# Performance work log

Hardware: AMD Instinct MI355X
Metric: run time of the kernel (lower is better)

The kernel has to match this reference:

```python
import jax, jax.numpy as jnp
import numpy as np

B, SQ, SKV, D = 8, 2048, 2048, 1024

def setup_inputs() -> dict:
    key = jax.random.key(0)
    ks = jax.random.split(key, 8)
    s = 1.0 / np.sqrt(D)  # torch Linear default init range
    return {
        "target": jax.random.normal(ks[0], (B, SQ, D), dtype=jnp.float32),
        "non_target": jax.random.normal(ks[1], (B, SKV, D), dtype=jnp.float32),
        "Wq": jax.random.uniform(ks[2], (D, D), jnp.float32, -s, s),
        "bq": jax.random.uniform(ks[3], (D,), jnp.float32, -s, s),
        "Wk": jax.random.uniform(ks[4], (D, D), jnp.float32, -s, s),
        "bk": jax.random.uniform(ks[5], (D,), jnp.float32, -s, s),
        "Wv": jax.random.uniform(ks[6], (D, D), jnp.float32, -s, s),
        "bv": jax.random.uniform(ks[7], (D,), jnp.float32, -s, s),
    }

def reference(target, non_target, Wq, bq, Wk, bk, Wv, bv):
    # Linear projections (torch Linear: x @ W.T + b)
    q = jnp.einsum('bsd,ed->bse', target, Wq) + bq       # [B,SQ,D]
    k = jnp.einsum('bsd,ed->bse', non_target, Wk) + bk   # [B,SKV,D]
    v = jnp.einsum('bsd,ed->bse', non_target, Wv) + bv   # [B,SKV,D]
    # Unscaled attention, exactly as the original module (no 1/sqrt(d))
    scores = jnp.einsum('bqd,bkd->bqk', q, k)            # [B,SQ,SKV]
    weights = jax.nn.softmax(scores, axis=-1)
    return jnp.einsum('bqk,bkd->bqd', weights, v)        # [B,SQ,D]
```

## Files before the change

kernel.cpp:

```cpp
#include <hip/hip_runtime.h>


typedef _Float16 half8 __attribute__((ext_vector_type(8)));
typedef _Float16 half4v __attribute__((ext_vector_type(4)));
typedef float floatx4 __attribute__((ext_vector_type(4)));

__device__ __forceinline__ void async_copy16(const _Float16* g, _Float16* l) {
  __builtin_amdgcn_global_load_lds(
      (const __attribute__((address_space(1))) void*)g,
      (__attribute__((address_space(3))) void*)l,
      16, 0, 0);
}

__global__ __launch_bounds__(256) void cast_f32_f16(const float* __restrict__ src,
                                                    _Float16* __restrict__ dst, long n) {
  long i = ((long)blockIdx.x * 256 + threadIdx.x) * 8;
  if (i >= n) return;
  float4 a = *(const float4*)(src + i);
  float4 b = *(const float4*)(src + i + 4);
  half8 h;
  h[0] = (_Float16)a.x; h[1] = (_Float16)a.y; h[2] = (_Float16)a.z; h[3] = (_Float16)a.w;
  h[4] = (_Float16)b.x; h[5] = (_Float16)b.y; h[6] = (_Float16)b.z; h[7] = (_Float16)b.w;
  *(half8*)(dst + i) = h;
}

template <int OMODE>
__global__ __launch_bounds__(256, 2) void gemm_bt(const _Float16* __restrict__ A,
                                                  const _Float16* __restrict__ B,
                                                  const float* __restrict__ bias,
                                                  void* __restrict__ out,
                                                  int K, int N,
                                                  long sA, long sB, long sO) {
  __shared__ __attribute__((aligned(16))) _Float16 As[128 * 32];
  __shared__ __attribute__((aligned(16))) _Float16 Bs[128 * 32];

  const int tid = threadIdx.x;
  const int lane = tid & 63;
  const int wave = tid >> 6;
  const long bz = blockIdx.z;

  const _Float16* Ab = A + bz * sA + (long)blockIdx.x * 128 * K;
  const _Float16* Bb = B + bz * sB + (long)blockIdx.y * 128 * K;

  const int wm = (wave & 1) * 64;
  const int wn = (wave >> 1) * 64;
  const int frow = lane & 15;
  const int fq = lane >> 4;

  floatx4 acc[4][4];
#pragma unroll
  for (int mt = 0; mt < 4; mt++)
#pragma unroll
    for (int nt = 0; nt < 4; nt++)
      acc[mt][nt] = (floatx4){0.f, 0.f, 0.f, 0.f};

  const int c0 = tid, c1 = tid + 256;
  const int ar0 = c0 >> 2, ao0 = (c0 & 3) * 8;
  const int ar1 = c1 >> 2, ao1 = (c1 & 3) * 8;

  for (int k0 = 0; k0 < K; k0 += 32) {
    __syncthreads();
    async_copy16(Ab + (long)ar0 * K + k0 + ao0, As + c0 * 8);
    async_copy16(Ab + (long)ar1 * K + k0 + ao1, As + c1 * 8);
    async_copy16(Bb + (long)ar0 * K + k0 + ao0, Bs + c0 * 8);
    async_copy16(Bb + (long)ar1 * K + k0 + ao1, Bs + c1 * 8);
    __syncthreads();

    half8 af[4], bf[4];
#pragma unroll
    for (int mt = 0; mt < 4; mt++)
      af[mt] = *(const half8*)(As + (wm + mt * 16 + frow) * 32 + fq * 8);
#pragma unroll
    for (int nt = 0; nt < 4; nt++)
      bf[nt] = *(const half8*)(Bs + (wn + nt * 16 + frow) * 32 + fq * 8);
#pragma unroll
    for (int mt = 0; mt < 4; mt++)
#pragma unroll
      for (int nt = 0; nt < 4; nt++)
        acc[mt][nt] = __builtin_amdgcn_mfma_f32_16x16x32_f16(af[mt], bf[nt], acc[mt][nt], 0, 0, 0);
  }

  if (OMODE == 2) {
    float* O = (float*)out + bz * sO;
#pragma unroll
    for (int nt = 0; nt < 4; nt++) {
      const int n = blockIdx.y * 128 + wn + nt * 16 + frow;
#pragma unroll
      for (int mt = 0; mt < 4; mt++) {
        const int rbase = blockIdx.x * 128 + wm + mt * 16 + fq * 4;
#pragma unroll
        for (int i = 0; i < 4; i++)
          O[(long)(rbase + i) * N + n] = acc[mt][nt][i];
      }
    }
  } else {
#pragma unroll
    for (int nt = 0; nt < 4; nt++) {
      const int n = blockIdx.y * 128 + wn + nt * 16 + frow;
      const float bv = bias[n];
#pragma unroll
      for (int mt = 0; mt < 4; mt++) {
        const int rbase = blockIdx.x * 128 + wm + mt * 16 + fq * 4;
#pragma unroll
        for (int i = 0; i < 4; i++) {
          const float v = acc[mt][nt][i] + bv;
          if (OMODE == 0) {
            ((_Float16*)out)[(long)(rbase + i) * N + n] = (_Float16)v;
          } else {
            const int r = rbase + i;
            const long bb = r >> 11;
            const int s = r & 2047;
            ((_Float16*)out)[bb * (2048l * 1024) + (long)n * 2048 + s] = (_Float16)v;
          }
        }
      }
    }
  }
}

__global__ __launch_bounds__(256) void softmax_rows(const float* __restrict__ S,
                                                    _Float16* __restrict__ P) {
  const long row = blockIdx.x;
  const float* src = S + row * 2048;
  _Float16* dst = P + row * 2048;
  const int tid = threadIdx.x;

  float4 v0 = ((const float4*)src)[tid];
  float4 v1 = ((const float4*)src)[tid + 256];

  float m = fmaxf(fmaxf(fmaxf(v0.x, v0.y), fmaxf(v0.z, v0.w)),
                  fmaxf(fmaxf(v1.x, v1.y), fmaxf(v1.z, v1.w)));
#pragma unroll
  for (int o = 32; o > 0; o >>= 1) m = fmaxf(m, __shfl_xor(m, o, 64));
  __shared__ float redm[4];
  if ((tid & 63) == 0) redm[tid >> 6] = m;
  __syncthreads();
  m = fmaxf(fmaxf(redm[0], redm[1]), fmaxf(redm[2], redm[3]));

  float e[8];
  e[0] = __expf(v0.x - m); e[1] = __expf(v0.y - m);
  e[2] = __expf(v0.z - m); e[3] = __expf(v0.w - m);
  e[4] = __expf(v1.x - m); e[5] = __expf(v1.y - m);
  e[6] = __expf(v1.z - m); e[7] = __expf(v1.w - m);
  float s = ((e[0] + e[1]) + (e[2] + e[3])) + ((e[4] + e[5]) + (e[6] + e[7]));
#pragma unroll
  for (int o = 32; o > 0; o >>= 1) s += __shfl_xor(s, o, 64);
  __shared__ float reds[4];
  if ((tid & 63) == 0) reds[tid >> 6] = s;
  __syncthreads();
  s = (reds[0] + reds[1]) + (reds[2] + reds[3]);
  const float inv = 1.f / s;

  half4v h0, h1;
  h0[0] = (_Float16)(e[0] * inv); h0[1] = (_Float16)(e[1] * inv);
  h0[2] = (_Float16)(e[2] * inv); h0[3] = (_Float16)(e[3] * inv);
  h1[0] = (_Float16)(e[4] * inv); h1[1] = (_Float16)(e[5] * inv);
  h1[2] = (_Float16)(e[6] * inv); h1[3] = (_Float16)(e[7] * inv);
  *(half4v*)(dst + tid * 4) = h0;
  *(half4v*)(dst + 1024 + tid * 4) = h1;
}

extern "C" void kernel_launch(void* const* d_in, const int* in_sizes, int n_in,
                              void* d_out, int out_size, void* d_ws, size_t ws_size,
                              hipStream_t stream) {
  const float* target = (const float*)d_in[0];
  const float* non_target = (const float*)d_in[1];
  const float* Wq = (const float*)d_in[2];
  const float* bq = (const float*)d_in[3];
  const float* Wk = (const float*)d_in[4];
  const float* bk = (const float*)d_in[5];
  const float* Wv = (const float*)d_in[6];
  const float* bv = (const float*)d_in[7];

  char* ws = (char*)d_ws;
  const size_t MB = 1ull << 20;
  _Float16* tgt16 = (_Float16*)(ws);
  _Float16* ntg16 = (_Float16*)(ws + 32 * MB);
  float* S = (float*)(ws);
  _Float16* Q16 = (_Float16*)(ws + 128 * MB);
  _Float16* K16 = (_Float16*)(ws + 160 * MB);
  _Float16* P16 = (_Float16*)(ws + 128 * MB);
  _Float16* Vt16 = (_Float16*)(ws + 192 * MB);
  _Float16* Wq16 = (_Float16*)(ws + 224 * MB);
  _Float16* Wk16 = (_Float16*)(ws + 226 * MB);
  _Float16* Wv16 = (_Float16*)(ws + 228 * MB);

  const long nBig = 8l * 2048 * 1024;
  const long nW = 1024l * 1024;

  cast_f32_f16<<<8192, 256, 0, stream>>>(target, tgt16, nBig);
  cast_f32_f16<<<8192, 256, 0, stream>>>(non_target, ntg16, nBig);
  cast_f32_f16<<<512, 256, 0, stream>>>(Wq, Wq16, nW);
  cast_f32_f16<<<512, 256, 0, stream>>>(Wk, Wk16, nW);
  cast_f32_f16<<<512, 256, 0, stream>>>(Wv, Wv16, nW);

  gemm_bt<0><<<dim3(128, 8, 1), 256, 0, stream>>>(tgt16, Wq16, bq, Q16, 1024, 1024, 0, 0, 0);
  gemm_bt<0><<<dim3(128, 8, 1), 256, 0, stream>>>(ntg16, Wk16, bk, K16, 1024, 1024, 0, 0, 0);
  gemm_bt<1><<<dim3(128, 8, 1), 256, 0, stream>>>(ntg16, Wv16, bv, Vt16, 1024, 1024, 0, 0, 0);

  gemm_bt<2><<<dim3(16, 16, 8), 256, 0, stream>>>(Q16, K16, nullptr, S, 1024, 2048,
                                                  2048l * 1024, 2048l * 1024, 2048l * 2048);

  softmax_rows<<<16384, 256, 0, stream>>>(S, P16);

  gemm_bt<2><<<dim3(16, 8, 8), 256, 0, stream>>>(P16, Vt16, nullptr, (float*)d_out, 2048, 1024,
                                                 2048l * 2048, 1024l * 2048, 2048l * 1024);
}
```

Before: 541.1 us.

## Double GEMM K-tile with XOR-swizzled LDS, store scores in fp16, vectorize stores

The GEMM K-step grows from 32 to 64, with an XOR swizzle on the LDS layout to avoid bank conflicts on fragment reads, which halves the number of barrier pairs per K. The attention score matrix is now written in fp16 instead of fp32, halving its write and read traffic between the QK GEMM and the softmax. The transposed V epilogue stores half4 vectors, and the softmax reads and writes half8. The cost is more LDS per block and fp16 rounding of the unscaled scores, which can be large in magnitude and may lose precision or overflow before the softmax.

```diff
diff --git a/kernel.cpp b/kernel.cpp
--- a/kernel.cpp
+++ b/kernel.cpp
@@ -31,8 +31,8 @@
                                                   void* __restrict__ out,
                                                   int K, int N,
                                                   long sA, long sB, long sO) {
-  __shared__ __attribute__((aligned(16))) _Float16 As[128 * 32];
-  __shared__ __attribute__((aligned(16))) _Float16 Bs[128 * 32];
+  __shared__ __attribute__((aligned(16))) _Float16 As[128 * 64];
+  __shared__ __attribute__((aligned(16))) _Float16 Bs[128 * 64];
 
   const int tid = threadIdx.x;
   const int lane = tid & 63;
@@ -46,6 +46,7 @@
   const int wn = (wave >> 1) * 64;
   const int frow = lane & 15;
   const int fq = lane >> 4;
+  const int fsw = frow & 7;
 
   floatx4 acc[4][4];
 #pragma unroll
@@ -54,34 +55,38 @@
     for (int nt = 0; nt < 4; nt++)
       acc[mt][nt] = (floatx4){0.f, 0.f, 0.f, 0.f};
 
-  const int c0 = tid, c1 = tid + 256;
-  const int ar0 = c0 >> 2, ao0 = (c0 & 3) * 8;
-  const int ar1 = c1 >> 2, ao1 = (c1 & 3) * 8;
-
-  for (int k0 = 0; k0 < K; k0 += 32) {
+  const int sr = tid >> 3;
+  const int gl = (tid & 7) ^ (sr & 7);
+  const long gOffBase = (long)sr * K + gl * 8;
+  const int ldsOff = tid * 8;
+
+  for (int k0 = 0; k0 < K; k0 += 64) {
     __syncthreads();
-    async_copy16(Ab + (long)ar0 * K + k0 + ao0, As + c0 * 8);
-    async_copy16(Ab + (long)ar1 * K + k0 + ao1, As + c1 * 8);
-    async_copy16(Bb + (long)ar0 * K + k0 + ao0, Bs + c0 * 8);
-    async_copy16(Bb + (long)ar1 * K + k0 + ao1, Bs + c1 * 8);
+#pragma unroll
+    for (int j = 0; j < 4; j++) {
+      async_copy16(Ab + gOffBase + (long)(32 * j) * K + k0, As + ldsOff + j * 2048);
+      async_copy16(Bb + gOffBase + (long)(32 * j) * K + k0, Bs + ldsOff + j * 2048);
+    }
     __syncthreads();
 
-    half8 af[4], bf[4];
-#pragma unroll
-    for (int mt = 0; mt < 4; mt++)
-      af[mt] = *(const half8*)(As + (wm + mt * 16 + frow) * 32 + fq * 8);
-#pragma unroll
-    for (int nt = 0; nt < 4; nt++)
-      bf[nt] = *(const half8*)(Bs + (wn + nt * 16 + frow) * 32 + fq * 8);
-#pragma unroll
-    for (int mt = 0; mt < 4; mt++)
+#pragma unroll
+    for (int h = 0; h < 2; h++) {
+      half8 af[4], bf[4];
+#pragma unroll
+      for (int mt = 0; mt < 4; mt++)
+        af[mt] = *(const half8*)(As + (wm + mt * 16 + frow) * 64 + ((h * 4 + fq) ^ fsw) * 8);
 #pragma unroll
       for (int nt = 0; nt < 4; nt++)
-        acc[mt][nt] = __builtin_amdgcn_mfma_f32_16x16x32_f16(af[mt], bf[nt], acc[mt][nt], 0, 0, 0);
+        bf[nt] = *(const half8*)(Bs + (wn + nt * 16 + frow) * 64 + ((h * 4 + fq) ^ fsw) * 8);
+#pragma unroll
+      for (int mt = 0; mt < 4; mt++)
+#pragma unroll
+        for (int nt = 0; nt < 4; nt++)
+          acc[mt][nt] = __builtin_amdgcn_mfma_f32_16x16x32_f16(af[mt], bf[nt], acc[mt][nt], 0, 0, 0);
+    }
   }
 
-  if (OMODE == 2) {
-    float* O = (float*)out + bz * sO;
+  if (OMODE == 2 || OMODE == 3) {
 #pragma unroll
     for (int nt = 0; nt < 4; nt++) {
       const int n = blockIdx.y * 128 + wn + nt * 16 + frow;
@@ -89,47 +94,53 @@
       for (int mt = 0; mt < 4; mt++) {
         const int rbase = blockIdx.x * 128 + wm + mt * 16 + fq * 4;
 #pragma unroll
-        for (int i = 0; i < 4; i++)
-          O[(long)(rbase + i) * N + n] = acc[mt][nt][i];
+        for (int i = 0; i < 4; i++) {
+          if (OMODE == 2)
+            ((float*)out + bz * sO)[(long)(rbase + i) * N + n] = acc[mt][nt][i];
+          else
+            ((_Float16*)out + bz * sO)[(long)(rbase + i) * N + n] = (_Float16)acc[mt][nt][i];
+        }
       }
     }
   } else {
 #pragma unroll
     for (int nt = 0; nt < 4; nt++) {
       const int n = blockIdx.y * 128 + wn + nt * 16 + frow;
-      const float bv = bias[n];
+      const float bvv = bias[n];
 #pragma unroll
       for (int mt = 0; mt < 4; mt++) {
         const int rbase = blockIdx.x * 128 + wm + mt * 16 + fq * 4;
-#pragma unroll
-        for (int i = 0; i < 4; i++) {
-          const float v = acc[mt][nt][i] + bv;
-          if (OMODE == 0) {
-            ((_Float16*)out)[(long)(rbase + i) * N + n] = (_Float16)v;
-          } else {
-            const int r = rbase + i;
-            const long bb = r >> 11;
-            const int s = r & 2047;
-            ((_Float16*)out)[bb * (2048l * 1024) + (long)n * 2048 + s] = (_Float16)v;
-          }
+        if (OMODE == 0) {
+#pragma unroll
+          for (int i = 0; i < 4; i++)
+            ((_Float16*)out)[(long)(rbase + i) * N + n] = (_Float16)(acc[mt][nt][i] + bvv);
+        } else {
+          const long bb = rbase >> 11;
+          const int s = rbase & 2047;
+          half4v hv;
+#pragma unroll
+          for (int i = 0; i < 4; i++) hv[i] = (_Float16)(acc[mt][nt][i] + bvv);
+          *(half4v*)((_Float16*)out + bb * (2048l * 1024) + (long)n * 2048 + s) = hv;
         }
       }
     }
   }
 }
 
-__global__ __launch_bounds__(256) void softmax_rows(const float* __restrict__ S,
+__global__ __launch_bounds__(256) void softmax_rows(const _Float16* __restrict__ S,
                                                     _Float16* __restrict__ P) {
   const long row = blockIdx.x;
-  const float* src = S + row * 2048;
+  const _Float16* src = S + row * 2048;
   _Float16* dst = P + row * 2048;
   const int tid = threadIdx.x;
 
-  float4 v0 = ((const float4*)src)[tid];
-  float4 v1 = ((const float4*)src)[tid + 256];
-
-  float m = fmaxf(fmaxf(fmaxf(v0.x, v0.y), fmaxf(v0.z, v0.w)),
-                  fmaxf(fmaxf(v1.x, v1.y), fmaxf(v1.z, v1.w)));
+  half8 v = ((const half8*)src)[tid];
+  float f[8];
+#pragma unroll
+  for (int i = 0; i < 8; i++) f[i] = (float)v[i];
+
+  float m = fmaxf(fmaxf(fmaxf(f[0], f[1]), fmaxf(f[2], f[3])),
+                  fmaxf(fmaxf(f[4], f[5]), fmaxf(f[6], f[7])));
 #pragma unroll
   for (int o = 32; o > 0; o >>= 1) m = fmaxf(m, __shfl_xor(m, o, 64));
   __shared__ float redm[4];
@@ -137,12 +148,9 @@
   __syncthreads();
   m = fmaxf(fmaxf(redm[0], redm[1]), fmaxf(redm[2], redm[3]));
 
-  float e[8];
-  e[0] = __expf(v0.x - m); e[1] = __expf(v0.y - m);
-  e[2] = __expf(v0.z - m); e[3] = __expf(v0.w - m);
-  e[4] = __expf(v1.x - m); e[5] = __expf(v1.y - m);
-  e[6] = __expf(v1.z - m); e[7] = __expf(v1.w - m);
-  float s = ((e[0] + e[1]) + (e[2] + e[3])) + ((e[4] + e[5]) + (e[6] + e[7]));
+  float e[8], s = 0.f;
+#pragma unroll
+  for (int i = 0; i < 8; i++) { e[i] = __expf(f[i] - m); s += e[i]; }
 #pragma unroll
   for (int o = 32; o > 0; o >>= 1) s += __shfl_xor(s, o, 64);
   __shared__ float reds[4];
@@ -151,13 +159,10 @@
   s = (reds[0] + reds[1]) + (reds[2] + reds[3]);
   const float inv = 1.f / s;
 
-  half4v h0, h1;
-  h0[0] = (_Float16)(e[0] * inv); h0[1] = (_Float16)(e[1] * inv);
-  h0[2] = (_Float16)(e[2] * inv); h0[3] = (_Float16)(e[3] * inv);
-  h1[0] = (_Float16)(e[4] * inv); h1[1] = (_Float16)(e[5] * inv);
-  h1[2] = (_Float16)(e[6] * inv); h1[3] = (_Float16)(e[7] * inv);
-  *(half4v*)(dst + tid * 4) = h0;
-  *(half4v*)(dst + 1024 + tid * 4) = h1;
+  half8 h;
+#pragma unroll
+  for (int i = 0; i < 8; i++) h[i] = (_Float16)(e[i] * inv);
+  ((half8*)dst)[tid] = h;
 }
 
 extern "C" void kernel_launch(void* const* d_in, const int* in_sizes, int n_in,
@@ -176,10 +181,10 @@
   const size_t MB = 1ull << 20;
   _Float16* tgt16 = (_Float16*)(ws);
   _Float16* ntg16 = (_Float16*)(ws + 32 * MB);
-  float* S = (float*)(ws);
+  _Float16* S16 = (_Float16*)(ws);
+  _Float16* P16 = (_Float16*)(ws + 64 * MB);
   _Float16* Q16 = (_Float16*)(ws + 128 * MB);
   _Float16* K16 = (_Float16*)(ws + 160 * MB);
-  _Float16* P16 = (_Float16*)(ws + 128 * MB);
   _Float16* Vt16 = (_Float16*)(ws + 192 * MB);
   _Float16* Wq16 = (_Float16*)(ws + 224 * MB);
   _Float16* Wk16 = (_Float16*)(ws + 226 * MB);
@@ -198,10 +203,10 @@
   gemm_bt<0><<<dim3(128, 8, 1), 256, 0, stream>>>(ntg16, Wk16, bk, K16, 1024, 1024, 0, 0, 0);
   gemm_bt<1><<<dim3(128, 8, 1), 256, 0, stream>>>(ntg16, Wv16, bv, Vt16, 1024, 1024, 0, 0, 0);
 
-  gemm_bt<2><<<dim3(16, 16, 8), 256, 0, stream>>>(Q16, K16, nullptr, S, 1024, 2048,
+  gemm_bt<3><<<dim3(16, 16, 8), 256, 0, stream>>>(Q16, K16, nullptr, S16, 1024, 2048,
                                                   2048l * 1024, 2048l * 1024, 2048l * 2048);
 
-  softmax_rows<<<16384, 256, 0, stream>>>(S, P16);
+  softmax_rows<<<16384, 256, 0, stream>>>(S16, P16);
 
   gemm_bt<2><<<dim3(16, 8, 8), 256, 0, stream>>>(P16, Vt16, nullptr, (float*)d_out, 2048, 1024,
                                                  2048l * 2048, 1024l * 2048, 2048l * 1024);
```

After: 477.5 us. 1.13x faster.
